# Kernel optimization log

Hardware: AMD Instinct MI355X
Metric: run time of the kernel (lower is better)

The kernel has to match this reference:

```python
import jax, jax.numpy as jnp
import numpy as np

B, S, H = 2, 2048, 2048
NH, NKV, HD = 16, 4, 128
LAT = H // 8  # compression_ratio=8


def _rope_tables():
    inv_freq = 1.0 / (10000.0 ** (jnp.arange(0, HD, 2, dtype=jnp.float32) / HD))
    pos = jnp.arange(S, dtype=jnp.float32)
    freqs = pos[:, None] * inv_freq[None, :]          # [S, HD/2]
    emb = jnp.concatenate([freqs, freqs], axis=-1)    # [S, HD]
    return jnp.cos(emb)[None, None], jnp.sin(emb)[None, None]  # [1,1,S,HD]


def setup_inputs() -> dict:
    key = jax.random.key(0)
    ks = jax.random.split(key, 8)
    std = 0.02
    hidden_states = jax.random.normal(ks[0], (B, S, H), dtype=jnp.float32)
    cos, sin = _rope_tables()
    # additive causal mask, broadcast over batch/heads
    causal = jnp.tril(jnp.ones((S, S), dtype=bool))
    attention_mask = jnp.where(causal, 0.0, -1e9).astype(jnp.float32)[None, None]
    Wq = jax.random.normal(ks[1], (H, H), dtype=jnp.float32) * std
    Wk = jax.random.normal(ks[2], (NKV * HD, H), dtype=jnp.float32) * std
    Wv = jax.random.normal(ks[3], (NKV * HD, H), dtype=jnp.float32) * std
    Wo = jax.random.normal(ks[4], (H, H), dtype=jnp.float32) * std
    Wl_in = jax.random.normal(ks[5], (LAT, H), dtype=jnp.float32) * std
    Wl_out = jax.random.normal(ks[6], (H, LAT), dtype=jnp.float32) * std
    latent_gate = jnp.ones((1,), dtype=jnp.float32)
    return dict(hidden_states=hidden_states, cos=cos, sin=sin,
                attention_mask=attention_mask, Wq=Wq, Wk=Wk, Wv=Wv, Wo=Wo,
                Wl_in=Wl_in, Wl_out=Wl_out, latent_gate=latent_gate)


def _rotate_half(x):
    x1, x2 = jnp.split(x, 2, axis=-1)
    return jnp.concatenate([-x2, x1], axis=-1)


def reference(hidden_states, cos, sin, attention_mask, Wq, Wk, Wv, Wo,
              Wl_in, Wl_out, latent_gate):
    b, s, h = hidden_states.shape
    # projections (torch Linear: x @ W.T)
    q = (hidden_states @ Wq.T).reshape(b, s, NH, HD).transpose(0, 2, 1, 3)    # [b,nh,s,hd]
    k = (hidden_states @ Wk.T).reshape(b, s, NKV, HD).transpose(0, 2, 1, 3)   # [b,nkv,s,hd]
    v = (hidden_states @ Wv.T).reshape(b, s, NKV, HD).transpose(0, 2, 1, 3)
    # inline RoPE
    c, sn = cos[:, :, :s, :], sin[:, :, :s, :]
    q = q * c + _rotate_half(q) * sn
    k = k * c + _rotate_half(k) * sn
    # GQA: replicate kv heads (repeat_interleave along head dim)
    rep = NH // NKV
    k = jnp.repeat(k, rep, axis=1)
    v = jnp.repeat(v, rep, axis=1)
    scores = jnp.einsum('bhqd,bhkd->bhqk', q, k) / np.sqrt(HD).astype(np.float32)
    scores = scores + attention_mask
    attn = jax.nn.softmax(scores, axis=-1)
    ctx = jnp.einsum('bhqk,bhkd->bhqd', attn, v)          # [b,nh,s,hd]
    ctx = ctx.transpose(0, 2, 1, 3).reshape(b, s, h)
    attn_out = ctx @ Wo.T
    latent = (hidden_states @ Wl_in.T) @ Wl_out.T          # low-rank residual branch
    return attn_out + latent_gate * latent
```

## Files before the change

kernel.cpp:

```cpp
#include <hip/hip_runtime.h>
#include <hip/hip_bf16.h>

#define Bn   2
#define Sn   2048
#define Hn   2048
#define NHn  16
#define NKVn 4
#define HDn  128
#define LATn 256
#define Mn   (Bn*Sn)
#define KC   2304
#define NWn  3328

typedef unsigned short ushort_t;
typedef __attribute__((ext_vector_type(8))) short bf16x8;
typedef __attribute__((ext_vector_type(8))) unsigned short ushort8;
typedef __attribute__((ext_vector_type(4))) float f32x4;

__device__ __forceinline__ ushort_t f2bf(float f) {
    unsigned u = __float_as_uint(f);
    u += 0x7fffu + ((u >> 16) & 1u);
    return (ushort_t)(u >> 16);
}
__device__ __forceinline__ float bf2f(ushort_t h) {
    return __uint_as_float(((unsigned)h) << 16);
}
__device__ __forceinline__ void async16(const void* g, void* l) {
    __builtin_amdgcn_global_load_lds(
        (__attribute__((address_space(1))) void*)g,
        (__attribute__((address_space(3))) void*)l, 16, 0, 0);
}

struct CastArgs {
    const float* src[7];
    ushort_t*    dst[7];
    int n4[7];
    int sshift[7];
    int dcols[7];
    int dcoff[7];
};
__global__ __launch_bounds__(256)
void cast_fused(CastArgs a)
{
    int off = blockIdx.x * 256 + threadIdx.x;
    int seg = 0;
    while (seg < 6 && off >= a.n4[seg]) { off -= a.n4[seg]; ++seg; }
    const int r = off >> a.sshift[seg];
    const int c = off & ((1 << a.sshift[seg]) - 1);
    float4 f = ((const float4*)a.src[seg])[off];
    ushort4 o;
    o.x = f2bf(f.x); o.y = f2bf(f.y); o.z = f2bf(f.z); o.w = f2bf(f.w);
    ((ushort4*)a.dst[seg])[(size_t)r * a.dcols[seg] + a.dcoff[seg] + c] = o;
}

#define GEMM_BK64_LOOP(Aptr, Astr, Wptr, Wstr, Kdim)                          \
    for (int k0 = 0; k0 < (Kdim); k0 += 64) {                                 \
        _Pragma("unroll")                                                     \
        for (int it = 0; it < 4; ++it)                                        \
            async16((Aptr) + (size_t)(m0 + it*32 + srow)*(Astr) + k0 + scol,  \
                    As + (it*256 + tid)*8);                                   \
        _Pragma("unroll")                                                     \
        for (int it = 0; it < 4; ++it)                                        \
            async16((Wptr) + (size_t)(n0 + it*32 + srow)*(Wstr) + k0 + scol,  \
                    Bsm + (it*256 + tid)*8);                                  \
        __syncthreads();                                                      \
        _Pragma("unroll")                                                     \
        for (int hf = 0; hf < 2; ++hf) {                                      \
            bf16x8 af[4], bfr[4];                                             \
            _Pragma("unroll")                                                 \
            for (int mi = 0; mi < 4; ++mi)                                    \
                af[mi] = *(const bf16x8*)(As + aoff[hf*4 + mi]);              \
            _Pragma("unroll")                                                 \
            for (int ni = 0; ni < 4; ++ni)                                    \
                bfr[ni] = *(const bf16x8*)(Bsm + boff[hf*4 + ni]);            \
            _Pragma("unroll")                                                 \
            for (int mi = 0; mi < 4; ++mi)                                    \
                _Pragma("unroll")                                             \
                for (int ni = 0; ni < 4; ++ni)                                \
                    acc[mi][ni] = __builtin_amdgcn_mfma_f32_16x16x32_bf16(    \
                        af[mi], bfr[ni], acc[mi][ni], 0, 0, 0);               \
        }                                                                     \
        __syncthreads();                                                      \
    }

#define GEMM_COMMON_DECLS                                                     \
    const int tid  = threadIdx.x;                                             \
    const int lane = tid & 63, w = tid >> 6;                                  \
    const int t = lane & 15, q = lane >> 4;                                   \
    const int wm = w & 1, wn = w >> 1;                                        \
    const int srow = tid >> 3;                                                \
    const int scol = ((tid & 7) ^ ((tid >> 3) & 7)) * 8;                      \
    int aoff[8], boff[8];                                                     \
    _Pragma("unroll")                                                         \
    for (int hf = 0; hf < 2; ++hf)                                            \
        _Pragma("unroll")                                                     \
        for (int i = 0; i < 4; ++i) {                                         \
            aoff[hf*4 + i] = (wm*64 + i*16 + t)*64 + (((hf*4 + q) ^ (t & 7)) << 3); \
            boff[hf*4 + i] = (wn*64 + i*16 + t)*64 + (((hf*4 + q) ^ (t & 7)) << 3); \
        }                                                                     \
    f32x4 acc[4][4];                                                          \
    _Pragma("unroll")                                                         \
    for (int i = 0; i < 4; ++i)                                               \
        _Pragma("unroll")                                                     \
        for (int j = 0; j < 4; ++j) acc[i][j] = (f32x4){0.f, 0.f, 0.f, 0.f};

__global__ __launch_bounds__(256, 4)
void gemm_qkv(const ushort_t* __restrict__ A, const ushort_t* __restrict__ W,
              ushort_t* __restrict__ qo, ushort_t* __restrict__ ko,
              ushort_t* __restrict__ vo, ushort_t* __restrict__ ctxb,
              const float* __restrict__ gatep)
{
    __shared__ __align__(16) ushort_t smem[16384];
    ushort_t* As  = smem;
    ushort_t* Bsm = smem + 8192;

    const int m0 = blockIdx.y * 128, n0 = blockIdx.x * 128;
    GEMM_COMMON_DECLS
    GEMM_BK64_LOOP(A, Hn, W, Hn, Hn)

    const int bidx = m0 >> 11, s0 = m0 & (Sn - 1);

    if (n0 >= 2560 && n0 < 3072) {
        const int head = (n0 - 2560) >> 7;
        ushort_t* T = smem;
        #pragma unroll
        for (int h2 = 0; h2 < 2; ++h2) {
            __syncthreads();
            if (wn == h2) {
                #pragma unroll
                for (int mi = 0; mi < 4; ++mi)
                    #pragma unroll
                    for (int ni = 0; ni < 4; ++ni)
                        #pragma unroll
                        for (int r = 0; r < 4; ++r)
                            T[(wm*64 + mi*16 + q*4 + r)*64 + ni*16 + t] =
                                f2bf(acc[mi][ni][r]);
            }
            __syncthreads();
            const int dl = tid >> 2, tseg = (tid & 3) * 32;
            const size_t base =
                ((size_t)(bidx*NKVn + head)*HDn + h2*64 + dl) * Sn + s0 + tseg;
            #pragma unroll
            for (int j0 = 0; j0 < 4; ++j0) {
                ushort8 pk;
                #pragma unroll
                for (int u = 0; u < 8; ++u) pk[u] = T[(tseg + j0*8 + u)*64 + dl];
                *(ushort8*)(vo + base + j0*8) = pk;
            }
        }
        return;
    }

    ushort_t* obase;
    int rstride;
    float scale = 1.0f;
    if (n0 < 2048) {
        obase = qo + (((size_t)(bidx*NHn + (n0 >> 7)))*Sn + s0) * HDn;
        rstride = HDn;
    } else if (n0 < 2560) {
        obase = ko + (((size_t)(bidx*NKVn + ((n0 - 2048) >> 7)))*Sn + s0) * HDn;
        rstride = HDn;
    } else {
        obase = ctxb + (size_t)m0 * KC + (2048 + (n0 - 3072));
        rstride = KC;
        scale = gatep[0];
    }

    #pragma unroll
    for (int mi = 0; mi < 4; ++mi)
        #pragma unroll
        for (int r = 0; r < 4; ++r) {
            const int sl = wm*64 + mi*16 + q*4 + r;
            #pragma unroll
            for (int ni = 0; ni < 4; ++ni) {
                const int d = wn*64 + ni*16 + t;
                obase[(size_t)sl*rstride + d] = f2bf(scale * acc[mi][ni][r]);
            }
        }
}

__global__ __launch_bounds__(256, 4)
void gemm_out(const ushort_t* __restrict__ A, const ushort_t* __restrict__ W,
              float* __restrict__ outf)
{
    __shared__ __align__(16) ushort_t smem[16384];
    ushort_t* As  = smem;
    ushort_t* Bsm = smem + 8192;

    const int m0 = blockIdx.y * 128, n0 = blockIdx.x * 128;
    GEMM_COMMON_DECLS
    GEMM_BK64_LOOP(A, KC, W, KC, KC)

    #pragma unroll
    for (int mi = 0; mi < 4; ++mi)
        #pragma unroll
        for (int r = 0; r < 4; ++r) {
            const int m = m0 + wm*64 + mi*16 + q*4 + r;
            #pragma unroll
            for (int ni = 0; ni < 4; ++ni) {
                const int n = n0 + wn*64 + ni*16 + t;
                outf[(size_t)m * Hn + n] = acc[mi][ni][r];
            }
        }
}

__global__ __launch_bounds__(256)
void rope2_bf16(ushort_t* __restrict__ qx, ushort_t* __restrict__ kx,
                const float* __restrict__ cosb, const float* __restrict__ sinb)
{
    const int gid = blockIdx.x * 256 + threadIdx.x;
    const int row = gid >> 6, d = gid & 63;
    ushort_t* x; int r;
    if (row < Bn*NHn*Sn) { x = qx; r = row; }
    else                 { x = kx; r = row - Bn*NHn*Sn; }
    const int s = r & (Sn - 1);
    const float c0 = cosb[s*HDn + d],      c1 = cosb[s*HDn + d + 64];
    const float s0 = sinb[s*HDn + d],      s1 = sinb[s*HDn + d + 64];
    const size_t base = (size_t)r * HDn;
    const float x0 = bf2f(x[base + d]), x1 = bf2f(x[base + d + 64]);
    x[base + d]      = f2bf(x0*c0 - x1*s0);
    x[base + d + 64] = f2bf(x1*c1 + x0*s1);
}

__global__ __launch_bounds__(256)
void attn_mfma(const ushort_t* __restrict__ qg, const ushort_t* __restrict__ kg,
               const ushort_t* __restrict__ vtg, ushort_t* __restrict__ ctxb)
{
    __shared__ __align__(16) ushort_t Ks[2][8192];
    __shared__ __align__(16) ushort_t Vt[8192];
    __shared__ __align__(16) ushort_t Ps[4096];

    const int tid = threadIdx.x;
    const int w = tid >> 6, lane = tid & 63;
    const int t = lane & 15, q = lane >> 4;
    const int bh = blockIdx.y;
    const int b = bh >> 4, h = bh & 15;
    const int kvh = h >> 2;
    const ushort_t* qhead  = qg  + ((size_t)(b*NHn  + h  ))*Sn*HDn;
    const ushort_t* khead  = kg  + ((size_t)(b*NKVn + kvh))*Sn*HDn;
    const ushort_t* vthead = vtg + ((size_t)(b*NKVn + kvh))*HDn*Sn;

    const int ksr = tid >> 4;
    const int ksb = (tid & 15) ^ (ksr & 15);
    const int vtr = tid >> 3;
    const int vtb = (tid & 7) ^ (vtr & 7);

    int aqo[4], bko[16], vto[16], pso[16];
    #pragma unroll
    for (int ks = 0; ks < 4; ++ks)
        aqo[ks] = (w*16 + t)*128 + (((ks*4 + q) ^ t) << 3);
    #pragma unroll
    for (int nb = 0; nb < 4; ++nb)
        #pragma unroll
        for (int ks = 0; ks < 4; ++ks)
            bko[nb*4 + ks] = (nb*16 + t)*128 + (((ks*4 + q) ^ t) << 3);
    #pragma unroll
    for (int d2 = 0; d2 < 8; ++d2)
        #pragma unroll
        for (int ksp = 0; ksp < 2; ++ksp)
            vto[d2*2 + ksp] = (d2*16 + t)*64 + (((ksp*4 + q) ^ (t & 7)) << 3);
    #pragma unroll
    for (int nb = 0; nb < 4; ++nb)
        #pragma unroll
        for (int r = 0; r < 4; ++r) {
            const int row = q*4 + r;
            pso[nb*4 + r] = row*64 + (((nb*2 + (t >> 3)) ^ (row & 7)) << 3) + (t & 7);
        }

    const float cexp2 = 0.12751744737492532f;
    ushort_t* Pw = Ps + w*1024;
    const int apo0 = t*64 + ((q ^ (t & 7)) << 3);
    const int apo1 = t*64 + (((4 + q) ^ (t & 7)) << 3);

    for (int rep = 0; rep < 2; ++rep) {
        const int qt = rep ? (31 - (int)blockIdx.x) : (int)blockIdx.x;

        __syncthreads();
        #pragma unroll
        for (int it = 0; it < 4; ++it)
            async16(qhead + (size_t)(qt*64 + it*16 + ksr)*HDn + ksb*8,
                    Ks[0] + it*2048 + tid*8);
        __syncthreads();
        bf16x8 aq[4];
        #pragma unroll
        for (int ks = 0; ks < 4; ++ks) aq[ks] = *(const bf16x8*)(Ks[0] + aqo[ks]);
        __syncthreads();

        #pragma unroll
        for (int it = 0; it < 4; ++it)
            async16(khead + (size_t)(it*16 + ksr)*HDn + ksb*8,
                    Ks[0] + it*2048 + tid*8);
        __syncthreads();

        float l_lane[4] = {0.f, 0.f, 0.f, 0.f};
        f32x4 O[8];
        #pragma unroll
        for (int d2 = 0; d2 < 8; ++d2) O[d2] = (f32x4){0.f, 0.f, 0.f, 0.f};

        for (int kt = 0; kt <= qt; ++kt) {
            const ushort_t* Kc = Ks[kt & 1];
            ushort_t*       Kn = Ks[(kt & 1) ^ 1];

            #pragma unroll
            for (int it = 0; it < 4; ++it)
                async16(vthead + (size_t)(it*32 + vtr)*Sn + kt*64 + vtb*8,
                        Vt + it*2048 + tid*8);
            if (kt < qt) {
                #pragma unroll
                for (int it = 0; it < 4; ++it)
                    async16(khead + (size_t)((kt+1)*64 + it*16 + ksr)*HDn + ksb*8,
                            Kn + it*2048 + tid*8);
            }

            f32x4 sc[4];
            #pragma unroll
            for (int nb = 0; nb < 4; ++nb) {
                sc[nb] = (f32x4){0.f, 0.f, 0.f, 0.f};
                #pragma unroll
                for (int ks = 0; ks < 4; ++ks) {
                    bf16x8 bk = *(const bf16x8*)(Kc + bko[nb*4 + ks]);
                    sc[nb] = __builtin_amdgcn_mfma_f32_16x16x32_bf16(
                        aq[ks], bk, sc[nb], 0, 0, 0);
                }
            }

            float ps[4][4];
            if (kt == qt) {
                #pragma unroll
                for (int nb = 0; nb < 4; ++nb) {
                    const int kj = kt*64 + nb*16 + t;
                    #pragma unroll
                    for (int r = 0; r < 4; ++r) {
                        const int qi = qt*64 + w*16 + q*4 + r;
                        ps[nb][r] = (kj <= qi) ? exp2f(sc[nb][r]*cexp2) : 0.f;
                    }
                }
            } else {
                #pragma unroll
                for (int nb = 0; nb < 4; ++nb)
                    #pragma unroll
                    for (int r = 0; r < 4; ++r)
                        ps[nb][r] = exp2f(sc[nb][r]*cexp2);
            }
            #pragma unroll
            for (int nb = 0; nb < 4; ++nb)
                #pragma unroll
                for (int r = 0; r < 4; ++r) {
                    l_lane[r] += ps[nb][r];
                    Pw[pso[nb*4 + r]] = f2bf(ps[nb][r]);
                }

            __syncthreads();

            bf16x8 ap0 = *(const bf16x8*)(Pw + apo0);
            bf16x8 ap1 = *(const bf16x8*)(Pw + apo1);
            #pragma unroll
            for (int d2 = 0; d2 < 8; ++d2) {
                bf16x8 bv0 = *(const bf16x8*)(Vt + vto[d2*2 + 0]);
                O[d2] = __builtin_amdgcn_mfma_f32_16x16x32_bf16(ap0, bv0, O[d2], 0, 0, 0);
                bf16x8 bv1 = *(const bf16x8*)(Vt + vto[d2*2 + 1]);
                O[d2] = __builtin_amdgcn_mfma_f32_16x16x32_bf16(ap1, bv1, O[d2], 0, 0, 0);
            }
            __syncthreads();
        }

        float linv[4];
        #pragma unroll
        for (int r = 0; r < 4; ++r) {
            float lr = l_lane[r];
            lr += __shfl_xor(lr, 1);
            lr += __shfl_xor(lr, 2);
            lr += __shfl_xor(lr, 4);
            lr += __shfl_xor(lr, 8);
            linv[r] = 1.f / lr;
        }
        #pragma unroll
        for (int d2 = 0; d2 < 8; ++d2)
            #pragma unroll
            for (int r = 0; r < 4; ++r) {
                const size_t addr =
                    ((size_t)(b*Sn + qt*64 + w*16 + q*4 + r))*KC + h*HDn + d2*16 + t;
                ctxb[addr] = f2bf(O[d2][r] * linv[r]);
            }
    }
}

extern "C" void kernel_launch(void* const* d_in, const int* in_sizes, int n_in,
                              void* d_out, int out_size, void* d_ws, size_t ws_size,
                              hipStream_t stream)
{
    const float* hs    = (const float*)d_in[0];
    const float* cosb  = (const float*)d_in[1];
    const float* sinb  = (const float*)d_in[2];
    const float* Wq    = (const float*)d_in[4];
    const float* Wk    = (const float*)d_in[5];
    const float* Wv    = (const float*)d_in[6];
    const float* Wo    = (const float*)d_in[7];
    const float* Wlin  = (const float*)d_in[8];
    const float* Wlout = (const float*)d_in[9];
    const float* gate  = (const float*)d_in[10];
    float* out = (float*)d_out;

    ushort_t* p = (ushort_t*)d_ws;
    ushort_t* hsb    = p;  p += 8388608;
    ushort_t* Wqkvb  = p;  p += (size_t)NWn*2048;
    ushort_t* Wcomb  = p;  p += 2048*KC;
    ushort_t* qbb    = p;  p += 8388608;
    ushort_t* kbb    = p;  p += 2097152;
    ushort_t* vtb    = p;  p += 2097152;
    ushort_t* ctxc   = p;  p += (size_t)Mn*KC;

    const dim3 blk(256);

    {
        CastArgs ca;
        ca.src[0]=hs;    ca.dst[0]=hsb;                 ca.n4[0]=2097152; ca.sshift[0]=21; ca.dcols[0]=1<<21; ca.dcoff[0]=0;
        ca.src[1]=Wq;    ca.dst[1]=Wqkvb;               ca.n4[1]=1048576; ca.sshift[1]=20; ca.dcols[1]=1<<20; ca.dcoff[1]=0;
        ca.src[2]=Wk;    ca.dst[2]=Wqkvb + 2048*2048;   ca.n4[2]=262144;  ca.sshift[2]=18; ca.dcols[2]=1<<18; ca.dcoff[2]=0;
        ca.src[3]=Wv;    ca.dst[3]=Wqkvb + 2560*2048;   ca.n4[3]=262144;  ca.sshift[3]=18; ca.dcols[3]=1<<18; ca.dcoff[3]=0;
        ca.src[4]=Wlin;  ca.dst[4]=Wqkvb + 3072*2048;   ca.n4[4]=131072;  ca.sshift[4]=17; ca.dcols[4]=1<<17; ca.dcoff[4]=0;
        ca.src[5]=Wo;    ca.dst[5]=Wcomb;               ca.n4[5]=1048576; ca.sshift[5]=9;  ca.dcols[5]=576;   ca.dcoff[5]=0;
        ca.src[6]=Wlout; ca.dst[6]=Wcomb;               ca.n4[6]=131072;  ca.sshift[6]=6;  ca.dcols[6]=576;   ca.dcoff[6]=512;
        cast_fused<<<19456, blk, 0, stream>>>(ca);
    }

    gemm_qkv<<<dim3(26, 32), blk, 0, stream>>>(hsb, Wqkvb, qbb, kbb, vtb, ctxc, gate);

    rope2_bf16<<<((Bn*NHn*Sn + Bn*NKVn*Sn)*64)/256, blk, 0, stream>>>(qbb, kbb, cosb, sinb);

    attn_mfma<<<dim3(16, Bn*NHn), blk, 0, stream>>>(qbb, kbb, vtb, ctxc);

    gemm_out<<<dim3(16, 32), blk, 0, stream>>>(ctxc, Wcomb, out);
}
```

Baseline: 335.8 us.

## Keep attention probabilities in registers by computing transposed scores

The QK^T MFMA operands are swapped so each lane holds score values along the key dimension, which lets the probability tile be packed straight into the A operand of the PV MFMA with packed bf16 conversions. This removes the per-tile LDS round-trip for P and its shared buffer. The V-transpose writer in the projection kernel permutes the key order within each 32-key chunk to match the new register layout. The row-sum reduction becomes two lane shuffles plus a broadcast, at the cost of a more intricate layout coupling between the two kernels.

```diff
diff --git a/kernel.cpp b/kernel.cpp
--- a/kernel.cpp
+++ b/kernel.cpp
@@ -16,6 +16,7 @@
 typedef __attribute__((ext_vector_type(8))) short bf16x8;
 typedef __attribute__((ext_vector_type(8))) unsigned short ushort8;
 typedef __attribute__((ext_vector_type(4))) float f32x4;
+typedef __attribute__((ext_vector_type(4))) unsigned u32x4;
 
 __device__ __forceinline__ ushort_t f2bf(float f) {
     unsigned u = __float_as_uint(f);
@@ -24,6 +25,11 @@
 }
 __device__ __forceinline__ float bf2f(ushort_t h) {
     return __uint_as_float(((unsigned)h) << 16);
+}
+__device__ __forceinline__ unsigned cvt_pk_bf16(float lo, float hi) {
+    unsigned r;
+    asm("v_cvt_pk_bf16_f32 %0, %1, %2" : "=v"(r) : "v"(lo), "v"(hi));
+    return r;
 }
 __device__ __forceinline__ void async16(const void* g, void* l) {
     __builtin_amdgcn_global_load_lds(
@@ -144,7 +150,12 @@
             for (int j0 = 0; j0 < 4; ++j0) {
                 ushort8 pk;
                 #pragma unroll
-                for (int u = 0; u < 8; ++u) pk[u] = T[(tseg + j0*8 + u)*64 + dl];
+                for (int u = 0; u < 8; ++u) {
+                    const int p  = j0*8 + u;
+                    const int qg = (p >> 3) & 3, j = p & 7;
+                    const int orig = (j < 4) ? qg*4 + j : 16 + qg*4 + (j - 4);
+                    pk[u] = T[(tseg + orig)*64 + dl];
+                }
                 *(ushort8*)(vo + base + j0*8) = pk;
             }
         }
@@ -228,7 +239,6 @@
 {
     __shared__ __align__(16) ushort_t Ks[2][8192];
     __shared__ __align__(16) ushort_t Vt[8192];
-    __shared__ __align__(16) ushort_t Ps[4096];
 
     const int tid = threadIdx.x;
     const int w = tid >> 6, lane = tid & 63;
@@ -245,7 +255,7 @@
     const int vtr = tid >> 3;
     const int vtb = (tid & 7) ^ (vtr & 7);
 
-    int aqo[4], bko[16], vto[16], pso[16];
+    int aqo[4], bko[16], vto[16];
     #pragma unroll
     for (int ks = 0; ks < 4; ++ks)
         aqo[ks] = (w*16 + t)*128 + (((ks*4 + q) ^ t) << 3);
@@ -259,18 +269,8 @@
         #pragma unroll
         for (int ksp = 0; ksp < 2; ++ksp)
             vto[d2*2 + ksp] = (d2*16 + t)*64 + (((ksp*4 + q) ^ (t & 7)) << 3);
-    #pragma unroll
-    for (int nb = 0; nb < 4; ++nb)
-        #pragma unroll
-        for (int r = 0; r < 4; ++r) {
-            const int row = q*4 + r;
-            pso[nb*4 + r] = row*64 + (((nb*2 + (t >> 3)) ^ (row & 7)) << 3) + (t & 7);
-        }
 
     const float cexp2 = 0.12751744737492532f;
-    ushort_t* Pw = Ps + w*1024;
-    const int apo0 = t*64 + ((q ^ (t & 7)) << 3);
-    const int apo1 = t*64 + (((4 + q) ^ (t & 7)) << 3);
 
     for (int rep = 0; rep < 2; ++rep) {
         const int qt = rep ? (31 - (int)blockIdx.x) : (int)blockIdx.x;
@@ -292,7 +292,7 @@
                     Ks[0] + it*2048 + tid*8);
         __syncthreads();
 
-        float l_lane[4] = {0.f, 0.f, 0.f, 0.f};
+        float l_sum = 0.f;
         f32x4 O[8];
         #pragma unroll
         for (int d2 = 0; d2 < 8; ++d2) O[d2] = (f32x4){0.f, 0.f, 0.f, 0.f};
@@ -320,21 +320,20 @@
                 for (int ks = 0; ks < 4; ++ks) {
                     bf16x8 bk = *(const bf16x8*)(Kc + bko[nb*4 + ks]);
                     sc[nb] = __builtin_amdgcn_mfma_f32_16x16x32_bf16(
-                        aq[ks], bk, sc[nb], 0, 0, 0);
+                        bk, aq[ks], sc[nb], 0, 0, 0);
                 }
             }
 
             float ps[4][4];
             if (kt == qt) {
-                #pragma unroll
-                for (int nb = 0; nb < 4; ++nb) {
-                    const int kj = kt*64 + nb*16 + t;
+                const int qi = w*16 + t;
+                #pragma unroll
+                for (int nb = 0; nb < 4; ++nb)
                     #pragma unroll
                     for (int r = 0; r < 4; ++r) {
-                        const int qi = qt*64 + w*16 + q*4 + r;
+                        const int kj = nb*16 + q*4 + r;
                         ps[nb][r] = (kj <= qi) ? exp2f(sc[nb][r]*cexp2) : 0.f;
                     }
-                }
             } else {
                 #pragma unroll
                 for (int nb = 0; nb < 4; ++nb)
@@ -345,35 +344,41 @@
             #pragma unroll
             for (int nb = 0; nb < 4; ++nb)
                 #pragma unroll
-                for (int r = 0; r < 4; ++r) {
-                    l_lane[r] += ps[nb][r];
-                    Pw[pso[nb*4 + r]] = f2bf(ps[nb][r]);
-                }
+                for (int r = 0; r < 4; ++r)
+                    l_sum += ps[nb][r];
+
+            u32x4 pw0, pw1;
+            pw0[0] = cvt_pk_bf16(ps[0][0], ps[0][1]);
+            pw0[1] = cvt_pk_bf16(ps[0][2], ps[0][3]);
+            pw0[2] = cvt_pk_bf16(ps[1][0], ps[1][1]);
+            pw0[3] = cvt_pk_bf16(ps[1][2], ps[1][3]);
+            pw1[0] = cvt_pk_bf16(ps[2][0], ps[2][1]);
+            pw1[1] = cvt_pk_bf16(ps[2][2], ps[2][3]);
+            pw1[2] = cvt_pk_bf16(ps[3][0], ps[3][1]);
+            pw1[3] = cvt_pk_bf16(ps[3][2], ps[3][3]);
+            const bf16x8 pa0 = __builtin_bit_cast(bf16x8, pw0);
+            const bf16x8 pa1 = __builtin_bit_cast(bf16x8, pw1);
 
             __syncthreads();
 
-            bf16x8 ap0 = *(const bf16x8*)(Pw + apo0);
-            bf16x8 ap1 = *(const bf16x8*)(Pw + apo1);
             #pragma unroll
             for (int d2 = 0; d2 < 8; ++d2) {
                 bf16x8 bv0 = *(const bf16x8*)(Vt + vto[d2*2 + 0]);
-                O[d2] = __builtin_amdgcn_mfma_f32_16x16x32_bf16(ap0, bv0, O[d2], 0, 0, 0);
+                O[d2] = __builtin_amdgcn_mfma_f32_16x16x32_bf16(pa0, bv0, O[d2], 0, 0, 0);
                 bf16x8 bv1 = *(const bf16x8*)(Vt + vto[d2*2 + 1]);
-                O[d2] = __builtin_amdgcn_mfma_f32_16x16x32_bf16(ap1, bv1, O[d2], 0, 0, 0);
+                O[d2] = __builtin_amdgcn_mfma_f32_16x16x32_bf16(pa1, bv1, O[d2], 0, 0, 0);
             }
             __syncthreads();
         }
 
+        float lr = l_sum;
+        lr += __shfl_xor(lr, 16);
+        lr += __shfl_xor(lr, 32);
         float linv[4];
         #pragma unroll
-        for (int r = 0; r < 4; ++r) {
-            float lr = l_lane[r];
-            lr += __shfl_xor(lr, 1);
-            lr += __shfl_xor(lr, 2);
-            lr += __shfl_xor(lr, 4);
-            lr += __shfl_xor(lr, 8);
-            linv[r] = 1.f / lr;
-        }
+        for (int r = 0; r < 4; ++r)
+            linv[r] = 1.f / __shfl(lr, q*4 + r, 16);
+
         #pragma unroll
         for (int d2 = 0; d2 < 8; ++d2)
             #pragma unroll
```

After: 328.2 us. 2.3% less time.
